# Kernel tuning notes

Hardware: AMD Instinct MI355X
Metric: run time of the kernel (lower is better)

## Reference

```python
import jax, jax.numpy as jnp
import numpy as np

MODEL_DIM = 1024
HEADS = 16
HEAD_DIM = MODEL_DIM // HEADS
B, T = 2, 2048
TB_LEN = 500  # time_bias table length


def setup_inputs() -> dict:
    key = jax.random.key(0)
    ks = jax.random.split(key, 12)
    s = 0.02
    d = MODEL_DIM
    return {
        "x": jax.random.normal(ks[0], (B, T, d), dtype=jnp.float32),
        "Wq": jax.random.normal(ks[1], (d, d), dtype=jnp.float32) * s,
        "bq": jnp.zeros((d,), jnp.float32),
        "Wk": jax.random.normal(ks[2], (d, d), dtype=jnp.float32) * s,
        "bk": jnp.zeros((d,), jnp.float32),
        "Wv": jax.random.normal(ks[3], (d, d), dtype=jnp.float32) * s,
        "bv": jnp.zeros((d,), jnp.float32),
        "Wo": jax.random.normal(ks[4], (d, d), dtype=jnp.float32) * s,
        "bo": jnp.zeros((d,), jnp.float32),
        "et_gate": jax.random.normal(ks[5], (1, 1, 1), dtype=jnp.float32),
        "is_gate": jax.random.normal(ks[6], (1, 1, 1), dtype=jnp.float32),
        "time_bias": jnp.linspace(-1.0, 1.0, TB_LEN, dtype=jnp.float32).reshape(1, 1, TB_LEN),
    }


def reference(x, Wq, bq, Wk, bk, Wv, bv, Wo, bo, et_gate, is_gate, time_bias):
    Bb, Tt, D = x.shape
    H, hd = HEADS, HEAD_DIM
    # projections (torch Linear: y = x @ W.T + b), split heads -> [B,H,T,hd]
    Q = (x @ Wq.T + bq).reshape(Bb, Tt, H, hd).transpose(0, 2, 1, 3)
    K = (x @ Wk.T + bk).reshape(Bb, Tt, H, hd).transpose(0, 2, 1, 3)
    V = (x @ Wv.T + bv).reshape(Bb, Tt, H, hd).transpose(0, 2, 1, 3)
    scores = jnp.einsum("bhqd,bhkd->bhqk", Q, K) / jnp.sqrt(jnp.float32(hd))
    # relative-position gather from the fixed time-bias table
    pos = jnp.arange(Tt)[None, :] - jnp.arange(Tt)[:, None]          # [T,T]
    idx = jnp.clip(pos + TB_LEN // 2, 0, TB_LEN - 1)                 # [T,T]
    tp = time_bias[:, :, idx]                                        # [1,1,T,T]
    tp = jnp.squeeze(tp, axis=1)[None, None]                         # [1,1,1,T,T] (faithful to torch)
    # broadcast: [B,H,T,T] + [1,1,1,T,T] -> [1,B,H,T,T] (faithful 5-D scores)
    scores = scores + jax.nn.sigmoid(et_gate) * tp + is_gate
    attn = jax.nn.softmax(scores, axis=-1)                           # [1,B,H,T,T]
    context = jnp.matmul(attn, V)                                    # [1,B,H,T,hd]
    # faithful torch transpose(1,2).reshape(B,T,D) on the 5-D tensor
    context = context.transpose(0, 2, 1, 3, 4).reshape(Bb, Tt, D)
    return context @ Wo.T + bo
```

## Files before the change

### kernel.cpp

```cpp
#include <hip/hip_runtime.h>

typedef __bf16 bf16_t;
typedef __bf16 bf16x4 __attribute__((ext_vector_type(4)));
typedef __bf16 bf16x8 __attribute__((ext_vector_type(8)));
typedef float f32x4 __attribute__((ext_vector_type(4)));

__device__ __forceinline__ f32x4 mfma16(bf16x8 a, bf16x8 b, f32x4 c) {
    return __builtin_amdgcn_mfma_f32_16x16x32_bf16(a, b, c, 0, 0, 0);
}

__device__ __forceinline__ void gload16(bf16_t* lds, const bf16_t* g) {
    __builtin_amdgcn_global_load_lds(
        (const __attribute__((address_space(1))) void*)g,
        (__attribute__((address_space(3))) void*)lds, 16, 0, 0);
}

__device__ __forceinline__ bf16x4 trd(const bf16_t* p) {
    bf16x4 r;
    asm volatile("ds_read_b64_tr_b16 %0, %1"
                 : "=v"(r)
                 : "v"((const __attribute__((address_space(3))) bf16_t*)p));
    return r;
}

__device__ __forceinline__ float ex2(float x) {
    float r;
    asm("v_exp_f32 %0, %1" : "=v"(r) : "v"(x));
    return r;
}

__global__ __launch_bounds__(256) void cvt_all(
    const float* __restrict__ x,
    const float* __restrict__ w0, const float* __restrict__ w1,
    const float* __restrict__ w2, const float* __restrict__ w3,
    bf16_t* __restrict__ xb, bf16_t* __restrict__ o0, bf16_t* __restrict__ o1,
    bf16_t* __restrict__ o2, bf16_t* __restrict__ o3) {
    const int bid = blockIdx.x;
    const float* in;
    bf16_t* out;
    int off;
    if (bid < 4096) {
        in = x; out = xb; off = bid;
    } else {
        const int wsel = (bid - 4096) >> 10;
        off = (bid - 4096) & 1023;
        if (wsel == 0) { in = w0; out = o0; }
        else if (wsel == 1) { in = w1; out = o1; }
        else if (wsel == 2) { in = w2; out = o2; }
        else { in = w3; out = o3; }
    }
    const int i = (off * 256 + threadIdx.x) * 4;
    float4 v = *reinterpret_cast<const float4*>(in + i);
    bf16x4 o = {(bf16_t)v.x, (bf16_t)v.y, (bf16_t)v.z, (bf16_t)v.w};
    *reinterpret_cast<bf16x4*>(out + i) = o;
}

template <typename OutT>
__device__ __forceinline__ void gemm_tile(bf16_t (*As)[4096], bf16_t (*Bs)[4096],
                                          const bf16_t* A, const bf16_t* B,
                                          const float* bias, OutT* C,
                                          int M, int N, int K, int bx, int by,
                                          float scale) {
    const int tid = threadIdx.x;
    const int l = tid & 63, w = tid >> 6;
    const int lr = l & 15, lg = l >> 4;
    const int wr = (w >> 1) * 32, wc = (w & 1) * 64;
    const int m0 = bx * 128, n0 = by * 128;

    f32x4 acc[2][4];
#pragma unroll
    for (int m = 0; m < 2; ++m)
#pragma unroll
        for (int n = 0; n < 4; ++n) acc[m][n] = (f32x4)0.f;

    const int rA = tid >> 2, cA = (tid & 3) * 8;
    const bf16_t* ga = A + (size_t)(m0 + rA) * K + cA;
    const bf16_t* gb = B + (size_t)(n0 + rA) * K + cA;

    auto stage = [&](int buf) {
        gload16(As[buf] + tid * 8, ga);
        gload16(Bs[buf] + tid * 8, gb);
        ga += 32; gb += 32;
    };

    stage(0);
    stage(1);
    const int NT = K >> 5;
    int cur = 0, n2 = 2;
    for (int t = 0; t < NT; ++t) {
        if (t < NT - 1) asm volatile("s_waitcnt vmcnt(2)" ::: "memory");
        else asm volatile("s_waitcnt vmcnt(0)" ::: "memory");
        __builtin_amdgcn_sched_barrier(0);
        __builtin_amdgcn_s_barrier();
        __builtin_amdgcn_sched_barrier(0);
        if (t + 2 < NT) stage(n2);

        bf16x8 af[2], bfr[4];
#pragma unroll
        for (int m = 0; m < 2; ++m)
            af[m] = *reinterpret_cast<bf16x8*>(As[cur] + (wr + m * 16 + lr) * 32 + lg * 8);
#pragma unroll
        for (int n = 0; n < 4; ++n)
            bfr[n] = *reinterpret_cast<bf16x8*>(Bs[cur] + (wc + n * 16 + lr) * 32 + lg * 8);
#pragma unroll
        for (int m = 0; m < 2; ++m)
#pragma unroll
            for (int n = 0; n < 4; ++n)
                acc[m][n] = mfma16(af[m], bfr[n], acc[m][n]);

        cur = (cur == 2) ? 0 : cur + 1;
        n2 = (n2 == 2) ? 0 : n2 + 1;
    }
#pragma unroll
    for (int m = 0; m < 2; ++m) {
        const int row = m0 + wr + m * 16 + lg * 4;
#pragma unroll
        for (int n = 0; n < 4; ++n) {
            const int col = n0 + wc + n * 16 + lr;
            const float bv = bias[col];
#pragma unroll
            for (int j = 0; j < 4; ++j) {
                float v = (acc[m][n][j] + bv) * scale;
                C[(size_t)(row + j) * N + col] = (OutT)v;
            }
        }
    }
}

template <typename OutT>
__global__ __launch_bounds__(512, 4) void gemm_bt(const bf16_t* __restrict__ A,
                                                  const bf16_t* __restrict__ B,
                                                  const float* __restrict__ bias,
                                                  OutT* __restrict__ C,
                                                  int M, int N, int K) {
    __shared__ bf16_t As[3][4096];
    __shared__ bf16_t Bs[3][4096];
    gemm_tile<OutT>(As, Bs, A, B, bias, C, M, N, K, blockIdx.x, blockIdx.y, 1.f);
}

__global__ __launch_bounds__(512, 4) void gemm_qkv(
    const bf16_t* __restrict__ A,
    const bf16_t* W0, const bf16_t* W1, const bf16_t* W2,
    const float* b0, const float* b1, const float* b2,
    bf16_t* C0, bf16_t* C1, bf16_t* C2) {
    __shared__ bf16_t As[3][4096];
    __shared__ bf16_t Bs[3][4096];
    const bf16_t* B = W0; const float* bias = b0; bf16_t* C = C0;
    float scale = 0.1803368801111204f;
    if (blockIdx.z == 1) { B = W1; bias = b1; C = C1; scale = 1.f; }
    else if (blockIdx.z == 2) { B = W2; bias = b2; C = C2; scale = 1.f; }
    gemm_tile<bf16_t>(As, Bs, A, B, bias, C, 4096, 1024, 1024,
                      blockIdx.x, blockIdx.y, scale);
}

__global__ __launch_bounds__(256, 4) void attn_fused(
    const bf16_t* __restrict__ Qb, const bf16_t* __restrict__ Kb,
    const bf16_t* __restrict__ Vb, bf16_t* __restrict__ Cx,
    const float* __restrict__ time_bias, const float* __restrict__ et_gate) {
    constexpr int T = 2048;
    constexpr int D = 1024;
    __shared__ bf16_t Kl[2][4096];
    __shared__ bf16_t Vl[2][4096];
    const int tid = threadIdx.x;
    const int w = tid >> 6, l = tid & 63;
    const int lr = l & 15, lg = l >> 4;
    const int flat = blockIdx.x;
    const int xcd = flat & 7, idx = flat >> 3;
    const int bh = (xcd << 2) | (idx >> 5);
    const int qt = idx & 31;
    const int b = bh >> 4, h = bh & 15;
    const size_t bT = (size_t)b * T;
    const int h64 = h * 64;

    const float sig = 1.f / (1.f + __expf(-et_gate[0]));
    const float slope = (time_bias[499] - time_bias[0]) * (1.f / 499.f);
    const float c1 = sig * slope * 1.4426950408889634f;
    const float C499 = c1 * 499.f;

    const int q0 = qt * 64 + w * 16;
    const bf16_t* qbase = Qb + (bT + q0 + lr) * D + h64;
    bf16x8 qf0 = *reinterpret_cast<const bf16x8*>(qbase + lg * 8);
    bf16x8 qf1 = *reinterpret_cast<const bf16x8*>(qbase + 32 + lg * 8);

    const int r0 = tid >> 3, d80 = ((tid & 7) ^ (r0 & 7)) << 3;
    const int q1i = tid + 256;
    const int r1 = q1i >> 3, d81 = ((q1i & 7) ^ (r1 & 7)) << 3;
    const bf16_t* kg0 = Kb + (bT + r0) * D + h64 + d80;
    const bf16_t* kg1 = Kb + (bT + r1) * D + h64 + d81;
    const int kv0v = ((tid >> 5) << 2) + ((tid >> 1) & 3);
    const int dd0 = (((tid >> 3) & 3) << 4) + ((tid & 1) << 3);
    const int kv1v = ((q1i >> 5) << 2) + ((q1i >> 1) & 3);
    const int dd1 = (((q1i >> 3) & 3) << 4) + ((q1i & 1) << 3);
    const bf16_t* vg0 = Vb + (bT + kv0v) * D + h64 + dd0;
    const bf16_t* vg1 = Vb + (bT + kv1v) * D + h64 + dd1;

    auto stage = [&](int buf) {
        gload16(&Kl[buf][tid * 8], kg0);
        gload16(&Kl[buf][(tid + 256) * 8], kg1);
        gload16(&Vl[buf][tid * 8], vg0);
        gload16(&Vl[buf][(tid + 256) * 8], vg1);
        kg0 += 64 * D; kg1 += 64 * D; vg0 += 64 * D; vg1 += 64 * D;
    };

    f32x4 acc[4];
#pragma unroll
    for (int n = 0; n < 4; ++n) acc[n] = (f32x4)0.f;
    f32x4 acc_li = (f32x4)0.f;
    bf16x8 onesf;
#pragma unroll
    for (int e = 0; e < 8; ++e) onesf[e] = (bf16_t)1.f;

    float tb_lane = (float)(250 - q0 - lr + lg * 4);

    stage(0);
    const uint32_t swz = (uint32_t)(lr & 7) << 4;

    for (int t = 0; t < 32; ++t) {
        const int cur = t & 1;
        asm volatile("s_waitcnt vmcnt(2)" ::: "memory");
        __builtin_amdgcn_sched_barrier(0);
        __builtin_amdgcn_s_barrier();
        __builtin_amdgcn_sched_barrier(0);
        if (t < 31) stage(cur ^ 1);

        char* Kc = (char*)Kl[cur];

        f32x4 s[4];
#pragma unroll
        for (int n = 0; n < 4; ++n) {
            const uint32_t rowb = (uint32_t)(n * 16 + lr) * 128;
            bf16x8 kf0 = *reinterpret_cast<bf16x8*>(Kc + ((rowb + lg * 16) ^ swz));
            bf16x8 kf1 = *reinterpret_cast<bf16x8*>(Kc + ((rowb + 64 + lg * 16) ^ swz));
            s[n] = (f32x4)0.f;
            s[n] = mfma16(kf0, qf0, s[n]);
            s[n] = mfma16(kf1, qf1, s[n]);
        }

        const int base = 250 - q0 + t * 64;
        if (base >= 15 && base <= 436) {
#pragma unroll
            for (int n = 0; n < 4; ++n)
#pragma unroll
                for (int j = 0; j < 4; ++j) {
                    const float x = tb_lane + (float)(n * 16 + j);
                    s[n][j] = ex2(fmaf(c1, x, s[n][j]));
                }
        } else if (base + 63 <= 0) {
#pragma unroll
            for (int n = 0; n < 4; ++n)
#pragma unroll
                for (int j = 0; j < 4; ++j) s[n][j] = ex2(s[n][j]);
        } else if (base >= 514) {
#pragma unroll
            for (int n = 0; n < 4; ++n)
#pragma unroll
                for (int j = 0; j < 4; ++j) s[n][j] = ex2(s[n][j] + C499);
        } else {
#pragma unroll
            for (int n = 0; n < 4; ++n)
#pragma unroll
                for (int j = 0; j < 4; ++j) {
                    float x = tb_lane + (float)(n * 16 + j);
                    x = fminf(fmaxf(x, 0.f), 499.f);
                    s[n][j] = ex2(fmaf(c1, x, s[n][j]));
                }
        }
        tb_lane += 64.f;

        bf16x8 pf0, pf1;
#pragma unroll
        for (int j = 0; j < 4; ++j) {
            pf0[j] = (bf16_t)s[0][j];
            pf0[4 + j] = (bf16_t)s[1][j];
            pf1[j] = (bf16_t)s[2][j];
            pf1[4 + j] = (bf16_t)s[3][j];
        }

        if (t < 31) asm volatile("s_waitcnt vmcnt(4)" ::: "memory");
        else asm volatile("s_waitcnt vmcnt(0)" ::: "memory");
        __builtin_amdgcn_sched_barrier(0);
        __builtin_amdgcn_s_barrier();
        __builtin_amdgcn_sched_barrier(0);

        const bf16_t* vb2 = Vl[cur] + lg * 256 + lr * 4;
        bf16x4 vlo[8], vhi[8];
#pragma unroll
        for (int n = 0; n < 4; ++n)
#pragma unroll
            for (int c = 0; c < 2; ++c) {
                vlo[n * 2 + c] = trd(vb2 + c * 2048 + n * 64);
                vhi[n * 2 + c] = trd(vb2 + c * 2048 + 1024 + n * 64);
            }
        asm volatile("s_waitcnt lgkmcnt(0)" ::: "memory");
        __builtin_amdgcn_sched_barrier(0);

        acc_li = mfma16(pf0, onesf, acc_li);
        acc_li = mfma16(pf1, onesf, acc_li);
#pragma unroll
        for (int n = 0; n < 4; ++n)
#pragma unroll
            for (int c = 0; c < 2; ++c) {
                bf16x8 vf;
#pragma unroll
                for (int e = 0; e < 4; ++e) {
                    vf[e] = vlo[n * 2 + c][e];
                    vf[4 + e] = vhi[n * 2 + c][e];
                }
                acc[n] = mfma16(c ? pf1 : pf0, vf, acc[n]);
            }
        __builtin_amdgcn_sched_barrier(0);
    }

#pragma unroll
    for (int j = 0; j < 4; ++j) {
        const float invj = __builtin_amdgcn_rcpf(acc_li[j]);
        const int tq = q0 + lg * 4 + j;
        const size_t base_o = ((size_t)(h * 2 + b) * T + tq) * 64;
#pragma unroll
        for (int n = 0; n < 4; ++n)
            Cx[base_o + n * 16 + lr] = (bf16_t)(acc[n][j] * invj);
    }
}

extern "C" void kernel_launch(void* const* d_in, const int* in_sizes, int n_in,
                              void* d_out, int out_size, void* d_ws, size_t ws_size,
                              hipStream_t stream) {
    (void)in_sizes; (void)n_in; (void)out_size; (void)ws_size;
    const float* x  = (const float*)d_in[0];
    const float* Wq = (const float*)d_in[1];
    const float* bq = (const float*)d_in[2];
    const float* Wk = (const float*)d_in[3];
    const float* bk = (const float*)d_in[4];
    const float* Wv = (const float*)d_in[5];
    const float* bv = (const float*)d_in[6];
    const float* Wo = (const float*)d_in[7];
    const float* bo = (const float*)d_in[8];
    const float* et = (const float*)d_in[9];
    const float* tb = (const float*)d_in[11];

    char* ws = (char*)d_ws;
    const size_t MB = 1 << 20;
    bf16_t* xb  = (bf16_t*)(ws + 0 * MB);
    bf16_t* wqb = (bf16_t*)(ws + 8 * MB);
    bf16_t* wkb = (bf16_t*)(ws + 10 * MB);
    bf16_t* wvb = (bf16_t*)(ws + 12 * MB);
    bf16_t* wob = (bf16_t*)(ws + 14 * MB);
    bf16_t* Qb  = (bf16_t*)(ws + 16 * MB);
    bf16_t* Kb  = (bf16_t*)(ws + 24 * MB);
    bf16_t* Vb  = (bf16_t*)(ws + 32 * MB);
    bf16_t* Cx  = (bf16_t*)(ws + 40 * MB);

    cvt_all<<<8192, 256, 0, stream>>>(x, Wq, Wk, Wv, Wo, xb, wqb, wkb, wvb, wob);

    gemm_qkv<<<dim3(32, 8, 3), 512, 0, stream>>>(xb, wqb, wkb, wvb,
                                                 bq, bk, bv, Qb, Kb, Vb);

    attn_fused<<<1024, 256, 0, stream>>>(Qb, Kb, Vb, Cx, tb, et);

    gemm_bt<float><<<dim3(32, 8), 512, 0, stream>>>(Cx, wob, bo, (float*)d_out,
                                                    4096, 1024, 1024);
}
```

Baseline: 123.0 us.

## Triple-buffer K tiles to prefetch two steps ahead in attention loop

The K staging buffer grows from two to three slots, and K loads are now issued two iterations ahead while V stays double-buffered. The vmcnt waits are rebalanced to match the new in-flight counts. V transpose reads use immediate LDS offsets, and K fragment addresses are hoisted, which cuts per-iteration address arithmetic. The aim is to hide global-load latency better, at the cost of more LDS per block, which could reduce occupancy at 4 blocks per CU.

Result: faster. 119.5 us (-2.9%).

```diff
diff --git a/kernel.cpp b/kernel.cpp
--- a/kernel.cpp
+++ b/kernel.cpp
@@ -15,13 +15,10 @@
         (__attribute__((address_space(3))) void*)lds, 16, 0, 0);
 }
 
-__device__ __forceinline__ bf16x4 trd(const bf16_t* p) {
-    bf16x4 r;
-    asm volatile("ds_read_b64_tr_b16 %0, %1"
-                 : "=v"(r)
-                 : "v"((const __attribute__((address_space(3))) bf16_t*)p));
-    return r;
-}
+#define TRD(dst, base, OFFSTR)                                          \
+    asm volatile("ds_read_b64_tr_b16 %0, %1 offset:" OFFSTR             \
+                 : "=v"(dst)                                            \
+                 : "v"((const __attribute__((address_space(3))) bf16_t*)(base)))
 
 __device__ __forceinline__ float ex2(float x) {
     float r;
@@ -159,7 +156,7 @@
     const float* __restrict__ time_bias, const float* __restrict__ et_gate) {
     constexpr int T = 2048;
     constexpr int D = 1024;
-    __shared__ bf16_t Kl[2][4096];
+    __shared__ bf16_t Kl[3][4096];
     __shared__ bf16_t Vl[2][4096];
     const int tid = threadIdx.x;
     const int w = tid >> 6, l = tid & 63;
@@ -194,12 +191,15 @@
     const bf16_t* vg0 = Vb + (bT + kv0v) * D + h64 + dd0;
     const bf16_t* vg1 = Vb + (bT + kv1v) * D + h64 + dd1;
 
-    auto stage = [&](int buf) {
+    auto stageK = [&](int buf) {
         gload16(&Kl[buf][tid * 8], kg0);
         gload16(&Kl[buf][(tid + 256) * 8], kg1);
+        kg0 += 64 * D; kg1 += 64 * D;
+    };
+    auto stageV = [&](int buf) {
         gload16(&Vl[buf][tid * 8], vg0);
         gload16(&Vl[buf][(tid + 256) * 8], vg1);
-        kg0 += 64 * D; kg1 += 64 * D; vg0 += 64 * D; vg1 += 64 * D;
+        vg0 += 64 * D; vg1 += 64 * D;
     };
 
     f32x4 acc[4];
@@ -212,25 +212,35 @@
 
     float tb_lane = (float)(250 - q0 - lr + lg * 4);
 
-    stage(0);
+    stageK(0);
+    stageV(0);
+    stageK(1);
+
     const uint32_t swz = (uint32_t)(lr & 7) << 4;
+    const uint32_t koffA = (uint32_t)(lr * 128) + (((uint32_t)(lg * 16)) ^ swz);
+    const uint32_t koffB = (uint32_t)(lr * 128) + (((uint32_t)(64 + lg * 16)) ^ swz);
+    const int voff = lg * 256 + lr * 4;
+
+    int kcur = 0, vcur = 0;
 
     for (int t = 0; t < 32; ++t) {
-        const int cur = t & 1;
-        asm volatile("s_waitcnt vmcnt(2)" ::: "memory");
+        if (t < 31) asm volatile("s_waitcnt vmcnt(4)" ::: "memory");
+        else asm volatile("s_waitcnt vmcnt(2)" ::: "memory");
         __builtin_amdgcn_sched_barrier(0);
         __builtin_amdgcn_s_barrier();
         __builtin_amdgcn_sched_barrier(0);
-        if (t < 31) stage(cur ^ 1);
-
-        char* Kc = (char*)Kl[cur];
+        if (t + 2 < 32) stageK(kcur == 0 ? 2 : kcur - 1);
+        if (t + 1 < 32) stageV(vcur ^ 1);
+
+        const char* Kc = (const char*)Kl[kcur];
+        const char* Ka = Kc + koffA;
+        const char* Kb2 = Kc + koffB;
 
         f32x4 s[4];
 #pragma unroll
         for (int n = 0; n < 4; ++n) {
-            const uint32_t rowb = (uint32_t)(n * 16 + lr) * 128;
-            bf16x8 kf0 = *reinterpret_cast<bf16x8*>(Kc + ((rowb + lg * 16) ^ swz));
-            bf16x8 kf1 = *reinterpret_cast<bf16x8*>(Kc + ((rowb + 64 + lg * 16) ^ swz));
+            bf16x8 kf0 = *reinterpret_cast<const bf16x8*>(Ka + n * 2048);
+            bf16x8 kf1 = *reinterpret_cast<const bf16x8*>(Kb2 + n * 2048);
             s[n] = (f32x4)0.f;
             s[n] = mfma16(kf0, qf0, s[n]);
             s[n] = mfma16(kf1, qf1, s[n]);
@@ -276,39 +286,38 @@
             pf1[4 + j] = (bf16_t)s[3][j];
         }
 
-        if (t < 31) asm volatile("s_waitcnt vmcnt(4)" ::: "memory");
+        if (t < 30) asm volatile("s_waitcnt vmcnt(4)" ::: "memory");
+        else if (t == 30) asm volatile("s_waitcnt vmcnt(2)" ::: "memory");
         else asm volatile("s_waitcnt vmcnt(0)" ::: "memory");
         __builtin_amdgcn_sched_barrier(0);
         __builtin_amdgcn_s_barrier();
         __builtin_amdgcn_sched_barrier(0);
 
-        const bf16_t* vb2 = Vl[cur] + lg * 256 + lr * 4;
+        const bf16_t* vb2 = Vl[vcur] + voff;
         bf16x4 vlo[8], vhi[8];
-#pragma unroll
-        for (int n = 0; n < 4; ++n)
-#pragma unroll
-            for (int c = 0; c < 2; ++c) {
-                vlo[n * 2 + c] = trd(vb2 + c * 2048 + n * 64);
-                vhi[n * 2 + c] = trd(vb2 + c * 2048 + 1024 + n * 64);
-            }
+        TRD(vlo[0], vb2, "0");    TRD(vhi[0], vb2, "2048");
+        TRD(vlo[1], vb2, "4096"); TRD(vhi[1], vb2, "6144");
+        TRD(vlo[2], vb2, "128");  TRD(vhi[2], vb2, "2176");
+        TRD(vlo[3], vb2, "4224"); TRD(vhi[3], vb2, "6272");
+        TRD(vlo[4], vb2, "256");  TRD(vhi[4], vb2, "2304");
+        TRD(vlo[5], vb2, "4352"); TRD(vhi[5], vb2, "6400");
+        TRD(vlo[6], vb2, "384");  TRD(vhi[6], vb2, "2432");
+        TRD(vlo[7], vb2, "4480"); TRD(vhi[7], vb2, "6528");
         asm volatile("s_waitcnt lgkmcnt(0)" ::: "memory");
         __builtin_amdgcn_sched_barrier(0);
 
         acc_li = mfma16(pf0, onesf, acc_li);
         acc_li = mfma16(pf1, onesf, acc_li);
 #pragma unroll
-        for (int n = 0; n < 4; ++n)
-#pragma unroll
-            for (int c = 0; c < 2; ++c) {
-                bf16x8 vf;
-#pragma unroll
-                for (int e = 0; e < 4; ++e) {
-                    vf[e] = vlo[n * 2 + c][e];
-                    vf[4 + e] = vhi[n * 2 + c][e];
-                }
-                acc[n] = mfma16(c ? pf1 : pf0, vf, acc[n]);
-            }
-        __builtin_amdgcn_sched_barrier(0);
+        for (int i2 = 0; i2 < 8; ++i2) {
+            bf16x8 vf = __builtin_shufflevector(vlo[i2], vhi[i2],
+                                                0, 1, 2, 3, 4, 5, 6, 7);
+            acc[i2 >> 1] = mfma16((i2 & 1) ? pf1 : pf0, vf, acc[i2 >> 1]);
+        }
+        __builtin_amdgcn_sched_barrier(0);
+
+        kcur = (kcur == 2) ? 0 : kcur + 1;
+        vcur ^= 1;
     }
 
 #pragma unroll
```
